# Kernel optimization log

Hardware: AMD Instinct MI355X
Metric: run time of the kernel (lower is better)

The kernel has to match this reference:

```python
import jax, jax.numpy as jnp
import numpy as np

B, S, HID = 2, 2048, 2048
NH, NG = 32, 8
HD = HID // NH  # 64
KV = HD * NG    # 512


def setup_inputs() -> dict:
    key = jax.random.key(0)
    ks = jax.random.split(key, 9)
    w = lambda k, shp: jax.random.normal(k, shp, dtype=jnp.float32) * 0.02
    return {
        "hidden_state": jax.random.normal(ks[0], (B, S, HID), dtype=jnp.float32),
        "Wq": w(ks[1], (HID, HID)), "bq": jnp.zeros((HID,), jnp.float32),
        "Wk": w(ks[2], (HID, KV)),  "bk": jnp.zeros((KV,), jnp.float32),
        "Wv": w(ks[3], (HID, KV)),  "bv": jnp.zeros((KV,), jnp.float32),
        "Wo": w(ks[4], (HID, HID)), "bo": jnp.zeros((HID,), jnp.float32),
    }


def reference(hidden_state, Wq, bq, Wk, bk, Wv, bv, Wo, bo):
    bs, seq, _ = hidden_state.shape
    rep = NH // NG  # heads per KV group

    q = hidden_state @ Wq + bq                      # [B,S,HID]
    k = hidden_state @ Wk + bk                      # [B,S,KV]
    v = hidden_state @ Wv + bv

    q = q.reshape(bs, seq, NH, HD).transpose(0, 2, 1, 3)   # [B,NH,S,D]
    k = k.reshape(bs, seq, NG, HD).transpose(0, 2, 1, 3)   # [B,NG,S,D]
    v = v.reshape(bs, seq, NG, HD).transpose(0, 2, 1, 3)
    # grouped-KV expansion: each group repeated consecutively rep times
    k = jnp.repeat(k, rep, axis=1)                          # [B,NH,S,D]
    v = jnp.repeat(v, rep, axis=1)

    scores = jnp.einsum("bhqd,bhkd->bhqk", q, k) / jnp.sqrt(jnp.float32(HD))
    probs = jax.nn.softmax(scores, axis=-1)
    out = jnp.einsum("bhqk,bhkd->bhqd", probs, v)           # [B,NH,S,D]
    out = out.transpose(0, 2, 1, 3).reshape(bs, seq, HID)
    return out @ Wo + bo
```

## Files before the change

kernel.cpp:

```cpp
#include <hip/hip_runtime.h>
#include <hip/hip_bf16.h>
#include <math.h>

typedef __bf16 bf16x8 __attribute__((ext_vector_type(8)));
typedef float f32x4 __attribute__((ext_vector_type(4)));
typedef __hip_bfloat16 bf16_t;

#define MFMA_BF16(a, b, c) __builtin_amdgcn_mfma_f32_16x16x32_bf16((a), (b), (c), 0, 0, 0)

__device__ __forceinline__ void async_copy16(const bf16_t* g, bf16_t* lds_base) {
  __builtin_amdgcn_global_load_lds(
      (const __attribute__((address_space(1))) unsigned int*)g,
      (__attribute__((address_space(3))) unsigned int*)lds_base,
      16, 0, 0);
}

__device__ __forceinline__ unsigned fbits(float x) { return __builtin_bit_cast(unsigned, x); }

__global__ void cast_f32_to_bf16(const float* __restrict__ in, bf16_t* __restrict__ out, int n4) {
  int i = blockIdx.x * blockDim.x + threadIdx.x;
  if (i < n4) {
    float4 v = ((const float4*)in)[i];
    union { bf16_t h[4]; ushort4 u; } cv;
    cv.h[0] = __float2bfloat16(v.x);
    cv.h[1] = __float2bfloat16(v.y);
    cv.h[2] = __float2bfloat16(v.z);
    cv.h[3] = __float2bfloat16(v.w);
    ((ushort4*)out)[i] = cv.u;
  }
}

__global__ void concat_bias3(const float* __restrict__ bq, const float* __restrict__ bk,
                             const float* __restrict__ bv, float* __restrict__ dst, float qscale) {
  int i = blockIdx.x * blockDim.x + threadIdx.x;
  float v;
  if (i < 2048) v = bq[i] * qscale;
  else if (i < 2560) v = bk[i - 2048];
  else v = bv[i - 2560];
  dst[i] = v;
}

template <typename TIN>
__global__ void transpose_to_bf16(const TIN* __restrict__ in, bf16_t* __restrict__ out,
                                  int R, int C, int in_rs, size_t in_bs, size_t out_bs,
                                  float scale) {
  __shared__ float tile[32][33];
  in += (size_t)blockIdx.z * in_bs;
  out += (size_t)blockIdx.z * out_bs;
  const int c0 = blockIdx.x * 32, r0 = blockIdx.y * 32;
  const int tx = threadIdx.x, ty = threadIdx.y;
#pragma unroll
  for (int i = ty; i < 32; i += 8)
    tile[i][tx] = (float)in[(size_t)(r0 + i) * in_rs + c0 + tx];
  __syncthreads();
#pragma unroll
  for (int i = ty; i < 32; i += 8)
    out[(size_t)(c0 + i) * R + r0 + tx] = __float2bfloat16(tile[tx][i] * scale);
}

template <typename TOUT>
__global__ __launch_bounds__(256, 2) void gemm_bt(
    const bf16_t* __restrict__ A, const bf16_t* __restrict__ Bt,
    const float* __restrict__ bias, TOUT* __restrict__ C,
    int M, int N, int K) {
  __shared__ alignas(16) bf16_t As[128 * 32];
  __shared__ alignas(16) bf16_t Bs[128 * 32];

  const int tid = threadIdx.x;
  const int w = tid >> 6, lane = tid & 63;
  const int quad = lane >> 4, l16 = lane & 15;
  const int wm = w >> 1, wn = w & 1;
  const int m0 = blockIdx.y * 128, n0 = blockIdx.x * 128;

  f32x4 acc[4][4] = {};

  const int srow = lane >> 2;
  const int scol = (lane & 3) * 8;

  for (int k0 = 0; k0 < K; k0 += 32) {
#pragma unroll
    for (int c = 0; c < 2; ++c) {
      const int r = w * 32 + c * 16 + srow;
      async_copy16(A + (size_t)(m0 + r) * K + k0 + scol, &As[(w * 32 + c * 16) * 32]);
      async_copy16(Bt + (size_t)(n0 + r) * K + k0 + scol, &Bs[(w * 32 + c * 16) * 32]);
    }
    __syncthreads();

    bf16x8 af[4], bf[4];
#pragma unroll
    for (int i = 0; i < 4; ++i) {
      af[i] = *(const bf16x8*)&As[(wm * 64 + i * 16 + l16) * 32 + quad * 8];
      bf[i] = *(const bf16x8*)&Bs[(wn * 64 + i * 16 + l16) * 32 + quad * 8];
    }
#pragma unroll
    for (int i = 0; i < 4; ++i)
#pragma unroll
      for (int j = 0; j < 4; ++j)
        acc[i][j] = MFMA_BF16(af[i], bf[j], acc[i][j]);
    __syncthreads();
  }

#pragma unroll
  for (int i = 0; i < 4; ++i) {
    const int row = m0 + wm * 64 + i * 16 + quad * 4;
#pragma unroll
    for (int j = 0; j < 4; ++j) {
      const int col = n0 + wn * 64 + j * 16 + l16;
      const float bv = bias[col];
#pragma unroll
      for (int r = 0; r < 4; ++r) {
        const float val = acc[i][j][r] + bv;
        if constexpr (__is_same(TOUT, float)) {
          C[(size_t)(row + r) * N + col] = val;
        } else {
          C[(size_t)(row + r) * N + col] = __float2bfloat16(val);
        }
      }
    }
  }
}

__global__ __launch_bounds__(256, 4) void gqa_attn(
    const bf16_t* __restrict__ QKV, const bf16_t* __restrict__ VT, bf16_t* __restrict__ O) {
  constexpr int S = 2048, HID = 2048, QKVS = 3072, HD = 64;
  const int tid = threadIdx.x;
  const int w = tid >> 6, lane = tid & 63;
  const int quad = lane >> 4, l16 = lane & 15;
  const int q0 = blockIdx.x * 128;
  const int h = blockIdx.y, b = blockIdx.z;
  const int g = h >> 2;

  __shared__ alignas(16) bf16_t Ks[64 * 64];
  __shared__ alignas(16) bf16_t VTs[64 * 64];
  __shared__ alignas(16) bf16_t Ps[128 * 64];

  bf16x8 qf[2][2];
#pragma unroll
  for (int mt = 0; mt < 2; ++mt)
#pragma unroll
    for (int ks = 0; ks < 2; ++ks)
      qf[mt][ks] = *(const bf16x8*)&QKV[(size_t)(b * S + q0 + w * 32 + mt * 16 + l16) * QKVS +
                                        h * HD + ks * 32 + quad * 8];

  const int rr = lane >> 3, c7 = lane & 7;
  const int scol = (c7 ^ rr) * 8;
  const int sx = l16 & 7;

  const bf16_t* Kbase = QKV + (size_t)b * S * QKVS + 2048 + g * HD;
  const bf16_t* Vbase = VT + (size_t)(b * 512 + g * HD) * S;

  f32x4 oacc[2][4] = {};
  f32x4 lacc[2] = {};
  bf16x8 ones;
#pragma unroll
  for (int j = 0; j < 8; ++j) ones[j] = (__bf16)1.0f;

  for (int s0 = 0; s0 < S; s0 += 64) {
    __syncthreads();
#pragma unroll
    for (int cg = 0; cg < 2; ++cg) {
      const int r = w * 16 + cg * 8 + rr;
      async_copy16(Kbase + (size_t)(s0 + r) * QKVS + scol, &Ks[(w * 16 + cg * 8) * 64]);
      async_copy16(Vbase + (size_t)r * S + s0 + scol, &VTs[(w * 16 + cg * 8) * 64]);
    }
    __syncthreads();

#pragma unroll
    for (int nt = 0; nt < 4; ++nt) {
      bf16x8 kf0 = *(const bf16x8*)&Ks[(nt * 16 + l16) * 64 + ((quad ^ sx) * 8)];
      bf16x8 kf1 = *(const bf16x8*)&Ks[(nt * 16 + l16) * 64 + (((4 + quad) ^ sx) * 8)];
#pragma unroll
      for (int mt = 0; mt < 2; ++mt) {
        f32x4 s = {};
        s = MFMA_BF16(kf0, qf[mt][0], s);
        s = MFMA_BF16(kf1, qf[mt][1], s);
        const float p0 = __builtin_amdgcn_exp2f(s[0]);
        const float p1 = __builtin_amdgcn_exp2f(s[1]);
        const float p2 = __builtin_amdgcn_exp2f(s[2]);
        const float p3 = __builtin_amdgcn_exp2f(s[3]);
        uint2 pk;
        pk.x = __builtin_amdgcn_perm(fbits(p1), fbits(p0), 0x07060302);
        pk.y = __builtin_amdgcn_perm(fbits(p3), fbits(p2), 0x07060302);
        *(uint2*)&Ps[(w * 32 + mt * 16 + l16) * 64 +
                     (((nt * 2 + (quad >> 1)) ^ sx) * 8) + (quad & 1) * 4] = pk;
      }
    }

#pragma unroll
    for (int kc = 0; kc < 2; ++kc) {
      bf16x8 pf[2];
#pragma unroll
      for (int mt = 0; mt < 2; ++mt) {
        pf[mt] = *(const bf16x8*)&Ps[(w * 32 + mt * 16 + l16) * 64 + (((kc * 4 + quad) ^ sx) * 8)];
        lacc[mt] = MFMA_BF16(pf[mt], ones, lacc[mt]);
      }
#pragma unroll
      for (int dt = 0; dt < 4; ++dt) {
        bf16x8 vf = *(const bf16x8*)&VTs[(dt * 16 + l16) * 64 + (((kc * 4 + quad) ^ sx) * 8)];
#pragma unroll
        for (int mt = 0; mt < 2; ++mt)
          oacc[mt][dt] = MFMA_BF16(pf[mt], vf, oacc[mt][dt]);
      }
    }
  }

#pragma unroll
  for (int mt = 0; mt < 2; ++mt) {
    float linv[4];
#pragma unroll
    for (int r = 0; r < 4; ++r) linv[r] = 1.0f / lacc[mt][r];
#pragma unroll
    for (int dt = 0; dt < 4; ++dt)
#pragma unroll
      for (int r = 0; r < 4; ++r)
        O[(size_t)(b * S + q0 + w * 32 + mt * 16 + quad * 4 + r) * HID + h * HD + dt * 16 + l16] =
            __float2bfloat16(oacc[mt][dt][r] * linv[r]);
  }
}

extern "C" void kernel_launch(void* const* d_in, const int* in_sizes, int n_in,
                              void* d_out, int out_size, void* d_ws, size_t ws_size,
                              hipStream_t stream) {
  const float* hidden = (const float*)d_in[0];
  const float* Wq = (const float*)d_in[1];
  const float* bq = (const float*)d_in[2];
  const float* Wk = (const float*)d_in[3];
  const float* bk = (const float*)d_in[4];
  const float* Wv = (const float*)d_in[5];
  const float* bv = (const float*)d_in[6];
  const float* Wo = (const float*)d_in[7];
  const float* bo = (const float*)d_in[8];
  float* out = (float*)d_out;

  constexpr int B = 2, S = 2048, HID = 2048, KV = 512, QKVN = 3072;
  constexpr int M = B * S;
  const float c1 = 0.125f * 1.44269504089f;

  char* ws = (char*)d_ws;
  bf16_t* hiddenB = (bf16_t*)ws; ws += (size_t)M * HID * 2;
  bf16_t* WqkvT = (bf16_t*)ws;   ws += (size_t)QKVN * HID * 2;
  bf16_t* WoT = (bf16_t*)ws;     ws += (size_t)HID * HID * 2;
  bf16_t* qkv = (bf16_t*)ws;     ws += (size_t)M * QKVN * 2;
  bf16_t* vT = (bf16_t*)ws;      ws += (size_t)M * KV * 2;
  bf16_t* attn = (bf16_t*)ws;    ws += (size_t)M * HID * 2;
  float* bqkv = (float*)ws;      ws += QKVN * 4;

  dim3 tb(32, 8);
  cast_f32_to_bf16<<<(M * HID / 4 + 255) / 256, 256, 0, stream>>>(hidden, hiddenB, M * HID / 4);
  transpose_to_bf16<float><<<dim3(64, 64, 1), tb, 0, stream>>>(Wq, WqkvT, HID, HID, HID, 0, 0, c1);
  transpose_to_bf16<float><<<dim3(16, 64, 1), tb, 0, stream>>>(
      Wk, WqkvT + (size_t)2048 * HID, HID, KV, KV, 0, 0, 1.0f);
  transpose_to_bf16<float><<<dim3(16, 64, 1), tb, 0, stream>>>(
      Wv, WqkvT + (size_t)2560 * HID, HID, KV, KV, 0, 0, 1.0f);
  transpose_to_bf16<float><<<dim3(64, 64, 1), tb, 0, stream>>>(Wo, WoT, HID, HID, HID, 0, 0, 1.0f);
  concat_bias3<<<QKVN / 256, 256, 0, stream>>>(bq, bk, bv, bqkv, c1);

  gemm_bt<bf16_t><<<dim3(QKVN / 128, M / 128), 256, 0, stream>>>(hiddenB, WqkvT, bqkv, qkv, M, QKVN, HID);

  transpose_to_bf16<bf16_t><<<dim3(16, 64, 2), tb, 0, stream>>>(
      qkv + 2560, vT, S, KV, QKVN, (size_t)S * QKVN, (size_t)KV * S, 1.0f);

  gqa_attn<<<dim3(S / 128, 32, B), 256, 0, stream>>>(qkv, vT, attn);

  gemm_bt<float><<<dim3(HID / 128, M / 128), 256, 0, stream>>>(attn, WoT, bo, out, M, HID, HID);
}
```

Measured before the change: 330.8 us.

## Fuse prep kernels, write V transposed from QKV GEMM, double-buffer attention K/V

Merges the cast, four weight transposes and bias concat into one launch that dispatches on block index, cutting launch overhead. The QKV GEMM epilogue now writes the V columns directly in transposed layout, which removes the separate V transpose kernel and its extra pass over memory. The attention kernel double-buffers its K/V tiles so the next tile's async loads overlap compute. This raises LDS use and lowers the occupancy hint from 4 to 3 blocks.

```diff
diff --git a/kernel.cpp b/kernel.cpp
--- a/kernel.cpp
+++ b/kernel.cpp
@@ -17,51 +17,59 @@
 
 __device__ __forceinline__ unsigned fbits(float x) { return __builtin_bit_cast(unsigned, x); }
 
-__global__ void cast_f32_to_bf16(const float* __restrict__ in, bf16_t* __restrict__ out, int n4) {
-  int i = blockIdx.x * blockDim.x + threadIdx.x;
-  if (i < n4) {
-    float4 v = ((const float4*)in)[i];
+__global__ __launch_bounds__(256) void prep(
+    const float* __restrict__ hidden, const float* __restrict__ Wq, const float* __restrict__ Wk,
+    const float* __restrict__ Wv, const float* __restrict__ Wo,
+    const float* __restrict__ bq, const float* __restrict__ bk, const float* __restrict__ bv,
+    bf16_t* __restrict__ hiddenB, bf16_t* __restrict__ WqkvT, bf16_t* __restrict__ WoT,
+    float* __restrict__ bqkv, float c1) {
+  __shared__ float tile[32][33];
+  int bid = blockIdx.x;
+  const int t = threadIdx.x;
+  if (bid < 8192) {
+    const int i = bid * 256 + t;
+    float4 v = ((const float4*)hidden)[i];
     union { bf16_t h[4]; ushort4 u; } cv;
     cv.h[0] = __float2bfloat16(v.x);
     cv.h[1] = __float2bfloat16(v.y);
     cv.h[2] = __float2bfloat16(v.z);
     cv.h[3] = __float2bfloat16(v.w);
-    ((ushort4*)out)[i] = cv.u;
-  }
-}
-
-__global__ void concat_bias3(const float* __restrict__ bq, const float* __restrict__ bk,
-                             const float* __restrict__ bv, float* __restrict__ dst, float qscale) {
-  int i = blockIdx.x * blockDim.x + threadIdx.x;
-  float v;
-  if (i < 2048) v = bq[i] * qscale;
-  else if (i < 2560) v = bk[i - 2048];
-  else v = bv[i - 2560];
-  dst[i] = v;
-}
-
-template <typename TIN>
-__global__ void transpose_to_bf16(const TIN* __restrict__ in, bf16_t* __restrict__ out,
-                                  int R, int C, int in_rs, size_t in_bs, size_t out_bs,
-                                  float scale) {
-  __shared__ float tile[32][33];
-  in += (size_t)blockIdx.z * in_bs;
-  out += (size_t)blockIdx.z * out_bs;
-  const int c0 = blockIdx.x * 32, r0 = blockIdx.y * 32;
-  const int tx = threadIdx.x, ty = threadIdx.y;
+    ((ushort4*)hiddenB)[i] = cv.u;
+    return;
+  }
+  bid -= 8192;
+  if (bid >= 10240) {
+    const int i = (bid - 10240) * 256 + t;
+    float v;
+    if (i < 2048) v = bq[i] * c1;
+    else if (i < 2560) v = bk[i - 2048];
+    else v = bv[i - 2560];
+    bqkv[i] = v;
+    return;
+  }
+  const float* src;
+  bf16_t* dst;
+  int Cc, bx, by;
+  float scale = 1.0f;
+  if (bid < 4096) { src = Wq; dst = WqkvT; Cc = 2048; bx = bid & 63; by = bid >> 6; scale = c1; }
+  else if (bid < 5120) { bid -= 4096; src = Wk; dst = WqkvT + (size_t)2048 * 2048; Cc = 512; bx = bid & 15; by = bid >> 4; }
+  else if (bid < 6144) { bid -= 5120; src = Wv; dst = WqkvT + (size_t)2560 * 2048; Cc = 512; bx = bid & 15; by = bid >> 4; }
+  else { bid -= 6144; src = Wo; dst = WoT; Cc = 2048; bx = bid & 63; by = bid >> 6; }
+  const int tx = t & 31, ty = t >> 5;
+  const int c0 = bx * 32, r0 = by * 32;
 #pragma unroll
   for (int i = ty; i < 32; i += 8)
-    tile[i][tx] = (float)in[(size_t)(r0 + i) * in_rs + c0 + tx];
+    tile[i][tx] = src[(size_t)(r0 + i) * Cc + c0 + tx];
   __syncthreads();
 #pragma unroll
   for (int i = ty; i < 32; i += 8)
-    out[(size_t)(c0 + i) * R + r0 + tx] = __float2bfloat16(tile[tx][i] * scale);
+    dst[(size_t)(c0 + i) * 2048 + r0 + tx] = __float2bfloat16(tile[tx][i] * scale);
 }
 
 template <typename TOUT>
 __global__ __launch_bounds__(256, 2) void gemm_bt(
     const bf16_t* __restrict__ A, const bf16_t* __restrict__ Bt,
-    const float* __restrict__ bias, TOUT* __restrict__ C,
+    const float* __restrict__ bias, TOUT* __restrict__ C, bf16_t* __restrict__ vTp,
     int M, int N, int K) {
   __shared__ alignas(16) bf16_t As[128 * 32];
   __shared__ alignas(16) bf16_t Bs[128 * 32];
@@ -98,6 +106,24 @@
       for (int j = 0; j < 4; ++j)
         acc[i][j] = MFMA_BF16(af[i], bf[j], acc[i][j]);
     __syncthreads();
+  }
+
+  if (vTp != nullptr && n0 >= 2560) {
+#pragma unroll
+    for (int i = 0; i < 4; ++i) {
+      const int row = m0 + wm * 64 + i * 16 + quad * 4;
+      const int bb = row >> 11, s = row & 2047;
+#pragma unroll
+      for (int j = 0; j < 4; ++j) {
+        const int col = n0 + wn * 64 + j * 16 + l16;
+        const float bv = bias[col];
+        union { bf16_t h[4]; ushort4 u; } cv;
+#pragma unroll
+        for (int r = 0; r < 4; ++r) cv.h[r] = __float2bfloat16(acc[i][j][r] + bv);
+        *(ushort4*)&vTp[((size_t)bb * 512 + (col - 2560)) * 2048 + s] = cv.u;
+      }
+    }
+    return;
   }
 
 #pragma unroll
@@ -120,7 +146,7 @@
   }
 }
 
-__global__ __launch_bounds__(256, 4) void gqa_attn(
+__global__ __launch_bounds__(256, 3) void gqa_attn(
     const bf16_t* __restrict__ QKV, const bf16_t* __restrict__ VT, bf16_t* __restrict__ O) {
   constexpr int S = 2048, HID = 2048, QKVS = 3072, HD = 64;
   const int tid = threadIdx.x;
@@ -130,8 +156,8 @@
   const int h = blockIdx.y, b = blockIdx.z;
   const int g = h >> 2;
 
-  __shared__ alignas(16) bf16_t Ks[64 * 64];
-  __shared__ alignas(16) bf16_t VTs[64 * 64];
+  __shared__ alignas(16) bf16_t Ks[2][64 * 64];
+  __shared__ alignas(16) bf16_t VTs[2][64 * 64];
   __shared__ alignas(16) bf16_t Ps[128 * 64];
 
   bf16x8 qf[2][2];
@@ -155,20 +181,26 @@
 #pragma unroll
   for (int j = 0; j < 8; ++j) ones[j] = (__bf16)1.0f;
 
-  for (int s0 = 0; s0 < S; s0 += 64) {
-    __syncthreads();
+  auto stage = [&](int s0, int buf) {
 #pragma unroll
     for (int cg = 0; cg < 2; ++cg) {
       const int r = w * 16 + cg * 8 + rr;
-      async_copy16(Kbase + (size_t)(s0 + r) * QKVS + scol, &Ks[(w * 16 + cg * 8) * 64]);
-      async_copy16(Vbase + (size_t)r * S + s0 + scol, &VTs[(w * 16 + cg * 8) * 64]);
-    }
+      async_copy16(Kbase + (size_t)(s0 + r) * QKVS + scol, &Ks[buf][(w * 16 + cg * 8) * 64]);
+      async_copy16(Vbase + (size_t)r * S + s0 + scol, &VTs[buf][(w * 16 + cg * 8) * 64]);
+    }
+  };
+
+  stage(0, 0);
+
+  for (int it = 0; it < S / 64; ++it) {
+    const int cur = it & 1;
     __syncthreads();
+    if (it + 1 < S / 64) stage((it + 1) * 64, 1 - cur);
 
 #pragma unroll
     for (int nt = 0; nt < 4; ++nt) {
-      bf16x8 kf0 = *(const bf16x8*)&Ks[(nt * 16 + l16) * 64 + ((quad ^ sx) * 8)];
-      bf16x8 kf1 = *(const bf16x8*)&Ks[(nt * 16 + l16) * 64 + (((4 + quad) ^ sx) * 8)];
+      bf16x8 kf0 = *(const bf16x8*)&Ks[cur][(nt * 16 + l16) * 64 + ((quad ^ sx) * 8)];
+      bf16x8 kf1 = *(const bf16x8*)&Ks[cur][(nt * 16 + l16) * 64 + (((4 + quad) ^ sx) * 8)];
 #pragma unroll
       for (int mt = 0; mt < 2; ++mt) {
         f32x4 s = {};
@@ -196,7 +228,7 @@
       }
 #pragma unroll
       for (int dt = 0; dt < 4; ++dt) {
-        bf16x8 vf = *(const bf16x8*)&VTs[(dt * 16 + l16) * 64 + (((kc * 4 + quad) ^ sx) * 8)];
+        bf16x8 vf = *(const bf16x8*)&VTs[cur][(dt * 16 + l16) * 64 + (((kc * 4 + quad) ^ sx) * 8)];
 #pragma unroll
         for (int mt = 0; mt < 2; ++mt)
           oacc[mt][dt] = MFMA_BF16(pf[mt], vf, oacc[mt][dt]);
@@ -245,22 +277,14 @@
   bf16_t* attn = (bf16_t*)ws;    ws += (size_t)M * HID * 2;
   float* bqkv = (float*)ws;      ws += QKVN * 4;
 
-  dim3 tb(32, 8);
-  cast_f32_to_bf16<<<(M * HID / 4 + 255) / 256, 256, 0, stream>>>(hidden, hiddenB, M * HID / 4);
-  transpose_to_bf16<float><<<dim3(64, 64, 1), tb, 0, stream>>>(Wq, WqkvT, HID, HID, HID, 0, 0, c1);
-  transpose_to_bf16<float><<<dim3(16, 64, 1), tb, 0, stream>>>(
-      Wk, WqkvT + (size_t)2048 * HID, HID, KV, KV, 0, 0, 1.0f);
-  transpose_to_bf16<float><<<dim3(16, 64, 1), tb, 0, stream>>>(
-      Wv, WqkvT + (size_t)2560 * HID, HID, KV, KV, 0, 0, 1.0f);
-  transpose_to_bf16<float><<<dim3(64, 64, 1), tb, 0, stream>>>(Wo, WoT, HID, HID, HID, 0, 0, 1.0f);
-  concat_bias3<<<QKVN / 256, 256, 0, stream>>>(bq, bk, bv, bqkv, c1);
-
-  gemm_bt<bf16_t><<<dim3(QKVN / 128, M / 128), 256, 0, stream>>>(hiddenB, WqkvT, bqkv, qkv, M, QKVN, HID);
-
-  transpose_to_bf16<bf16_t><<<dim3(16, 64, 2), tb, 0, stream>>>(
-      qkv + 2560, vT, S, KV, QKVN, (size_t)S * QKVN, (size_t)KV * S, 1.0f);
+  prep<<<18444, 256, 0, stream>>>(hidden, Wq, Wk, Wv, Wo, bq, bk, bv,
+                                  hiddenB, WqkvT, WoT, bqkv, c1);
+
+  gemm_bt<bf16_t><<<dim3(QKVN / 128, M / 128), 256, 0, stream>>>(
+      hiddenB, WqkvT, bqkv, qkv, vT, M, QKVN, HID);
 
   gqa_attn<<<dim3(S / 128, 32, B), 256, 0, stream>>>(qkv, vT, attn);
 
-  gemm_bt<float><<<dim3(HID / 128, M / 128), 256, 0, stream>>>(attn, WoT, bo, out, M, HID, HID);
-}
+  gemm_bt<float><<<dim3(HID / 128, M / 128), 256, 0, stream>>>(
+      attn, WoT, bo, out, (bf16_t*)nullptr, M, HID, HID);
+}
```

After: 323.5 us. -2.2%, faster.
